# Optimization experiments

Hardware: AMD Instinct MI355X
Metric: run time of the kernel (lower is better)

The kernel has to match this reference:

```python
import jax, jax.numpy as jnp
import numpy as np

B, S, D = 2, 2048, 2048
H = 16
Q_LORA = 1024
KV_LORA = 512
NOPE = 128
ROPE = 64
VH = 128
QK = NOPE + ROPE
EPS = 1e-3
SCALE = QK ** -0.5


def rms_norm(x, w):
    x32 = x.astype(jnp.float32)
    n = x32 * jax.lax.rsqrt(jnp.mean(x32 * x32, axis=-1, keepdims=True) + EPS)
    return w * n.astype(x.dtype)


def apply_rope(x, cos, sin):
    # x: [b, s, h, d]; cos/sin: [1, s, 1, d//2].
    # torch view_as_complex pairs consecutive elements: (x0,x1),(x2,x3),...
    xr, xi = x[..., 0::2], x[..., 1::2]
    yr = xr * cos - xi * sin
    yi = xr * sin + xi * cos
    return jnp.stack([yr, yi], axis=-1).reshape(x.shape)


def setup_inputs() -> dict:
    key = jax.random.key(0)
    ks = jax.random.split(key, 8)

    def lin(k, out, inn):
        bound = 1.0 / float(np.sqrt(inn))
        return jax.random.uniform(k, (out, inn), jnp.float32, -bound, bound)

    inv_freq = 1.0 / (10000.0 ** (np.arange(0, ROPE, 2, dtype=np.float32) / ROPE))
    ang = np.arange(S, dtype=np.float32)[:, None] * inv_freq[None, :]  # [S, ROPE/2]
    return {
        "x": jax.random.normal(ks[0], (B, S, D), jnp.float32),
        "start_pos": 0,
        "cos": jnp.asarray(np.cos(ang), jnp.float32),
        "sin": jnp.asarray(np.sin(ang), jnp.float32),
        "wq_a_w": lin(ks[1], Q_LORA, D),
        "wq_a_b": jnp.zeros((Q_LORA,), jnp.float32),
        "q_norm_w": jnp.ones((Q_LORA,), jnp.float32),
        "wq_b_w": lin(ks[2], H * QK, Q_LORA),
        "wq_b_b": jnp.zeros((H * QK,), jnp.float32),
        "wkv_a_w": lin(ks[3], KV_LORA + ROPE, D),
        "wkv_a_b": jnp.zeros((KV_LORA + ROPE,), jnp.float32),
        "kv_norm_w": jnp.ones((KV_LORA,), jnp.float32),
        "wkv_b_w": lin(ks[4], H * (NOPE + VH), KV_LORA),
        "wo_w": lin(ks[5], D, H * VH),
        "wo_b": jnp.zeros((D,), jnp.float32),
    }


def reference(x, start_pos, cos, sin, wq_a_w, wq_a_b, q_norm_w, wq_b_w, wq_b_b,
              wkv_a_w, wkv_a_b, kv_norm_w, wkv_b_w, wo_w, wo_b):
    b, s, _ = x.shape
    cos_ = cos[None, :, None, :]
    sin_ = sin[None, :, None, :]

    # q path: low-rank down-proj, RMSNorm, up-proj
    q = rms_norm(x @ wq_a_w.T + wq_a_b, q_norm_w) @ wq_b_w.T + wq_b_b
    q = q.reshape(b, s, H, QK)
    q_nope, q_pe = q[..., :NOPE], q[..., NOPE:]
    q_pe = apply_rope(q_pe, cos_, sin_)

    # kv path: joint low-rank latent + rope key
    kv_full = x @ wkv_a_w.T + wkv_a_b
    kv, k_pe = kv_full[..., :KV_LORA], kv_full[..., KV_LORA:]
    k_pe = apply_rope(k_pe[:, :, None, :], cos_, sin_)[:, :, 0, :]  # [b, t, ROPE]

    wkv_b = wkv_b_w.reshape(H, NOPE + VH, KV_LORA)
    # absorb k up-projection into q (MLA trick): q_nope -> latent space
    q_nope = jnp.einsum('bshd,hdc->bshc', q_nope, wkv_b[:, :NOPE])  # [b,s,H,KV_LORA]

    kv_c = rms_norm(kv, kv_norm_w)  # latent KV cache contents [b, t, KV_LORA]

    scores = (jnp.einsum('bshc,btc->bsht', q_nope, kv_c)
              + jnp.einsum('bshr,btr->bsht', q_pe, k_pe)) * SCALE
    # NOTE: source builds a causal mask but never adds it -> plain softmax (faithful)
    probs = jax.nn.softmax(scores.astype(jnp.float32), axis=-1).astype(x.dtype)

    o = jnp.einsum('bsht,btc->bshc', probs, kv_c)          # latent output
    o = jnp.einsum('bshc,hdc->bshd', o, wkv_b[:, NOPE:])    # v up-projection
    return o.reshape(b, s, H * VH) @ wo_w.T + wo_b
```

## Files before the change

kernel.cpp:

```cpp
#include <hip/hip_runtime.h>
#include <stdint.h>

typedef uint16_t u16;
typedef __bf16 bf16x8 __attribute__((ext_vector_type(8)));
typedef float f32x4 __attribute__((ext_vector_type(4)));

#define EPS 1e-3f
#define SCALE_F 0.07216878364870323f
#define THR_RAW 110.0f

__device__ __forceinline__ float bf2f(u16 u) {
    union { uint32_t i; float f; } v; v.i = ((uint32_t)u) << 16; return v.f;
}
__device__ __forceinline__ u16 f2bf(float f) {
    union { float f; uint32_t i; } v; v.f = f;
    uint32_t x = v.i;
    return (u16)((x + 0x7fffu + ((x >> 16) & 1u)) >> 16);
}

__device__ __forceinline__ void async_cp16(const u16* g, u16* l) {
    __builtin_amdgcn_global_load_lds(
        (const __attribute__((address_space(1))) uint32_t*)g,
        (__attribute__((address_space(3))) uint32_t*)l,
        16, 0, 0);
}

struct Cvt {
    const void* src[14];
    u16* dst[14];
    long off[15];
};

__global__ __launch_bounds__(256) void cvt_kernel(Cvt c, const uint32_t* qnw_u32, long total8)
{
    const long i8 = (long)blockIdx.x * 256 + threadIdx.x;
    if (i8 >= total8) return;
    const long e = i8 * 8;
    const bool is_f32 = (qnw_u32[0] == 0x3F800000u);
    int t = 0;
    while (e >= c.off[t + 1]) ++t;
    const long local = e - c.off[t];
    u16* d = c.dst[t] + local;
    if (is_f32) {
        const float* s = (const float*)c.src[t] + local;
        #pragma unroll
        for (int j = 0; j < 8; ++j) d[j] = f2bf(s[j]);
    } else {
        const u16* s = (const u16*)c.src[t] + local;
        #pragma unroll
        for (int j = 0; j < 8; ++j) d[j] = s[j];
    }
}

__global__ __launch_bounds__(256) void gemm_bt_kernel(
    const u16* __restrict__ A, const u16* __restrict__ B,
    const u16* __restrict__ bias, u16* __restrict__ C,
    int M, int N, int K, int lda, int ldb, int ldc, float alpha, int c_f32,
    int z0, int hcnt,
    long sAl, long sAb, long sAh,
    long sBl, long sBb, long sBh,
    long sCl, long sCb, long sCh)
{
    const int zl = blockIdx.z;
    const int zg = z0 + zl;
    const int zb = zg / hcnt, zh = zg - zb * hcnt;
    A += (long)zl * sAl + (long)zb * sAb + (long)zh * sAh;
    B += (long)zl * sBl + (long)zb * sBb + (long)zh * sBh;
    C += (long)zl * sCl + (long)zb * sCb + (long)zh * sCh;

    __shared__ u16 As[128 * 64];
    __shared__ u16 Bs[128 * 64];

    const int tid  = threadIdx.x;
    const int wave = tid >> 6, lane = tid & 63;
    const int wm = (wave >> 1) << 6, wn = (wave & 1) << 6;
    const int quad = lane >> 4, r15 = lane & 15;

    const int tileM = blockIdx.y * 128;
    const int tileN = blockIdx.x * 128;

    const u16* Ag[4]; const u16* Bg[4];
    u16* lA[4]; u16* lB[4];
    #pragma unroll
    for (int i = 0; i < 4; ++i) {
        const int cc = i * 256 + tid;
        const int rA = cc >> 3, kb = (cc & 7) << 3;
        int rB = tileN + rA; if (rB > N - 1) rB = N - 1;
        Ag[i] = A + (long)(tileM + rA) * lda + kb;
        Bg[i] = B + (long)rB * ldb + kb;
        lA[i] = &As[cc << 3];
        lB[i] = &Bs[cc << 3];
    }

    f32x4 acc[4][4] = {};

    const u16* aRd[4]; const u16* bRd[4];
    #pragma unroll
    for (int i = 0; i < 4; ++i) {
        aRd[i] = &As[(wm + i * 16 + r15) * 64 + quad * 8];
        bRd[i] = &Bs[(wn + i * 16 + r15) * 64 + quad * 8];
    }

    for (int k0 = 0; k0 < K; k0 += 64) {
        #pragma unroll
        for (int i = 0; i < 4; ++i) {
            async_cp16(Ag[i], lA[i]);
            async_cp16(Bg[i], lB[i]);
            Ag[i] += 64; Bg[i] += 64;
        }
        __syncthreads();
        #pragma unroll
        for (int kk = 0; kk < 2; ++kk) {
            bf16x8 af[4], bfr[4];
            #pragma unroll
            for (int i = 0; i < 4; ++i) {
                af[i]  = *(const bf16x8*)(aRd[i] + kk * 32);
                bfr[i] = *(const bf16x8*)(bRd[i] + kk * 32);
            }
            #pragma unroll
            for (int mi = 0; mi < 4; ++mi)
                #pragma unroll
                for (int ni = 0; ni < 4; ++ni)
                    acc[mi][ni] = __builtin_amdgcn_mfma_f32_16x16x32_bf16(
                        af[mi], bfr[ni], acc[mi][ni], 0, 0, 0);
        }
        __syncthreads();
    }

    #pragma unroll
    for (int mi = 0; mi < 4; ++mi) {
        const int row = tileM + wm + mi * 16 + quad * 4;
        #pragma unroll
        for (int ni = 0; ni < 4; ++ni) {
            const int col = tileN + wn + ni * 16 + r15;
            if (col < N) {
                if (c_f32) {
                    const float bv = bias ? bf2f(bias[col]) : 0.f;
                    #pragma unroll
                    for (int r = 0; r < 4; ++r)
                        ((float*)C)[(long)(row + r) * ldc + col] =
                            acc[mi][ni][r] * alpha + bv;
                } else {
                    #pragma unroll
                    for (int r = 0; r < 4; ++r) {
                        u16 t = f2bf(acc[mi][ni][r] * alpha);
                        if (bias) t = f2bf(bf2f(t) + bf2f(bias[col]));
                        C[(long)(row + r) * ldc + col] = t;
                    }
                }
            }
        }
    }
}

#define PS 72

__global__ __launch_bounds__(256, 2) void flash_kernel(
    const u16* __restrict__ q, const u16* __restrict__ K2,
    const u16* __restrict__ Vt, u16* __restrict__ O)
{
    __shared__ __align__(16) u16 Ks[64 * 192];
    __shared__ __align__(16) u16 Vs[128 * 64];
    __shared__ __align__(16) u16 Ps[4][32 * PS];

    const int bid = blockIdx.x;
    const int xcd = bid & 7;
    const int idx = bid >> 3;
    const int bh  = xcd * 4 + (idx >> 4);
    const int mt  = idx & 15;
    const int b = bh >> 4, h = bh & 15;

    const int tid = threadIdx.x;
    const int wave = tid >> 6, lane = tid & 63;
    const int quad = lane >> 4, r15 = lane & 15;
    const int r7 = r15 & 7;

    const long qrow0 = (long)b * 2048 + mt * 128 + wave * 32;
    u16* myPs = Ps[wave];

    bf16x8 qf[2][6];
    #pragma unroll
    for (int mi = 0; mi < 2; ++mi) {
        const u16* qp = q + (qrow0 + mi * 16 + r15) * 3072 + h * 192 + quad * 8;
        #pragma unroll
        for (int kst = 0; kst < 6; ++kst)
            qf[mi][kst] = *(const bf16x8*)(qp + kst * 32);
    }

    f32x4 Oacc[2][8] = {};
    float m_i[2][4], l_i[2][4];
    #pragma unroll
    for (int mi = 0; mi < 2; ++mi)
        #pragma unroll
        for (int r = 0; r < 4; ++r) { m_i[mi][r] = -1e30f; l_i[mi][r] = 0.f; }

    const u16* Kbh = K2 + (long)b * 2048 * 3072 + h * 192;
    const u16* Vbh = Vt + (long)bh * 128 * 2048;

    const u16* gK[6];
    #pragma unroll
    for (int i = 0; i < 6; ++i) {
        const int c = i * 256 + tid;
        const int row = c / 24, s = c - row * 24;
        gK[i] = Kbh + (long)row * 3072 + ((s ^ (row & 7)) << 3);
    }
    const u16* gV[4];
    #pragma unroll
    for (int i = 0; i < 4; ++i) {
        const int c = i * 256 + tid;
        const int d = c >> 3, s = c & 7;
        gV[i] = Vbh + (long)d * 2048 + ((s ^ (d & 7)) << 3);
    }

    #pragma unroll
    for (int i = 0; i < 6; ++i) {
        async_cp16(gK[i], &Ks[(i * 256 + tid) << 3]);
        gK[i] += 64 * 3072;
    }
    __syncthreads();

    for (int j = 0; j < 32; ++j) {
        #pragma unroll
        for (int i = 0; i < 4; ++i) {
            async_cp16(gV[i], &Vs[(i * 256 + tid) << 3]);
            gV[i] += 64;
        }

        f32x4 S[2][4] = {};
        __builtin_amdgcn_s_setprio(1);
        #pragma unroll
        for (int kst = 0; kst < 6; ++kst) {
            bf16x8 bfr[4];
            #pragma unroll
            for (int ni = 0; ni < 4; ++ni)
                bfr[ni] = *(const bf16x8*)&Ks[(ni * 16 + r15) * 192
                                              + (((kst * 4 + quad) ^ r7) << 3)];
            #pragma unroll
            for (int mi = 0; mi < 2; ++mi)
                #pragma unroll
                for (int ni = 0; ni < 4; ++ni)
                    S[mi][ni] = __builtin_amdgcn_mfma_f32_16x16x32_bf16(
                        qf[mi][kst], bfr[ni], S[mi][ni], 0, 0, 0);
        }
        __builtin_amdgcn_s_setprio(0);

        __syncthreads();

        #pragma unroll
        for (int i = 0; i < 6; ++i) {
            async_cp16(gK[i], &Ks[(i * 256 + tid) << 3]);
            gK[i] += 64 * 3072;
        }

        float tmax[2][4];
        float gmax = -1e30f;
        #pragma unroll
        for (int mi = 0; mi < 2; ++mi)
            #pragma unroll
            for (int r = 0; r < 4; ++r) {
                float t = S[mi][0][r];
                #pragma unroll
                for (int ni = 1; ni < 4; ++ni) t = fmaxf(t, S[mi][ni][r]);
                t = fmaxf(t, __shfl_xor(t, 1, 16));
                t = fmaxf(t, __shfl_xor(t, 2, 16));
                t = fmaxf(t, __shfl_xor(t, 4, 16));
                t = fmaxf(t, __shfl_xor(t, 8, 16));
                tmax[mi][r] = t;
                gmax = fmaxf(gmax, t - m_i[mi][r]);
            }
        if (!__all(gmax <= THR_RAW)) {
            #pragma unroll
            for (int mi = 0; mi < 2; ++mi)
                #pragma unroll
                for (int r = 0; r < 4; ++r) {
                    const float mnew = fmaxf(m_i[mi][r], tmax[mi][r]);
                    const float al = __expf((m_i[mi][r] - mnew) * SCALE_F);
                    m_i[mi][r] = mnew;
                    l_i[mi][r] *= al;
                    #pragma unroll
                    for (int ni = 0; ni < 8; ++ni) Oacc[mi][ni][r] *= al;
                }
        }
        #pragma unroll
        for (int mi = 0; mi < 2; ++mi)
            #pragma unroll
            for (int r = 0; r < 4; ++r) {
                const int lrow = mi * 16 + quad * 4 + r;
                const float mm = m_i[mi][r];
                float ps = 0.f;
                #pragma unroll
                for (int ni = 0; ni < 4; ++ni) {
                    const float pv = __expf((S[mi][ni][r] - mm) * SCALE_F);
                    ps += pv;
                    myPs[lrow * PS + ni * 16 + r15] = f2bf(pv);
                }
                ps += __shfl_xor(ps, 1, 16);
                ps += __shfl_xor(ps, 2, 16);
                ps += __shfl_xor(ps, 4, 16);
                ps += __shfl_xor(ps, 8, 16);
                l_i[mi][r] += ps;
            }

        __builtin_amdgcn_s_setprio(1);
        #pragma unroll
        for (int kst = 0; kst < 2; ++kst) {
            bf16x8 af[2], bv[8];
            #pragma unroll
            for (int mi = 0; mi < 2; ++mi)
                af[mi] = *(const bf16x8*)&myPs[(mi * 16 + r15) * PS
                                               + kst * 32 + quad * 8];
            #pragma unroll
            for (int ni = 0; ni < 8; ++ni)
                bv[ni] = *(const bf16x8*)&Vs[(ni * 16 + r15) * 64
                                             + (((kst * 4 + quad) ^ r7) << 3)];
            #pragma unroll
            for (int mi = 0; mi < 2; ++mi)
                #pragma unroll
                for (int ni = 0; ni < 8; ++ni)
                    Oacc[mi][ni] = __builtin_amdgcn_mfma_f32_16x16x32_bf16(
                        af[mi], bv[ni], Oacc[mi][ni], 0, 0, 0);
        }
        __builtin_amdgcn_s_setprio(0);

        __syncthreads();
    }

    #pragma unroll
    for (int mi = 0; mi < 2; ++mi)
        #pragma unroll
        for (int r = 0; r < 4; ++r) {
            const float inv = 1.f / l_i[mi][r];
            const long row = qrow0 + mi * 16 + quad * 4 + r;
            #pragma unroll
            for (int ni = 0; ni < 8; ++ni)
                O[row * 2048 + h * 128 + ni * 16 + r15] =
                    f2bf(Oacc[mi][ni][r] * inv);
        }
}

__global__ __launch_bounds__(256) void rmsnorm_kernel(
    const u16* __restrict__ x, const u16* __restrict__ w, u16* __restrict__ y, int n)
{
    const long row = blockIdx.x;
    const u16* xr = x + row * n;
    u16* yr = y + row * n;
    const int tid = threadIdx.x;
    const int cnt = n >> 8;
    float v[4];
    float ss = 0.f;
    for (int i = 0; i < cnt; ++i) { v[i] = bf2f(xr[tid + (i << 8)]); ss += v[i] * v[i]; }
    for (int o = 32; o; o >>= 1) ss += __shfl_xor(ss, o, 64);
    __shared__ float sm[4];
    if ((tid & 63) == 0) sm[tid >> 6] = ss;
    __syncthreads();
    const float rinv = rsqrtf((sm[0] + sm[1] + sm[2] + sm[3]) / (float)n + EPS);
    for (int i = 0; i < cnt; ++i) {
        const u16 nb = f2bf(v[i] * rinv);
        yr[tid + (i << 8)] = f2bf(bf2f(w[tid + (i << 8)]) * bf2f(nb));
    }
}

__global__ __launch_bounds__(256) void kv_kernel(
    const u16* __restrict__ cosb, const u16* __restrict__ sinb,
    const u16* __restrict__ w, u16* __restrict__ kvf)
{
    const long bs = blockIdx.x;
    const int s = (int)(bs & 2047);
    u16* io = kvf + bs * 576;
    const int tid = threadIdx.x;
    const float v0 = bf2f(io[tid * 2]), v1 = bf2f(io[tid * 2 + 1]);
    float ss = v0 * v0 + v1 * v1;
    for (int off = 32; off; off >>= 1) ss += __shfl_xor(ss, off, 64);
    __shared__ float sm[4];
    if ((tid & 63) == 0) sm[tid >> 6] = ss;
    __syncthreads();
    const float rinv = rsqrtf((sm[0] + sm[1] + sm[2] + sm[3]) / 512.f + EPS);
    const u16 n0 = f2bf(v0 * rinv), n1 = f2bf(v1 * rinv);
    io[tid * 2]     = f2bf(bf2f(w[tid * 2]) * bf2f(n0));
    io[tid * 2 + 1] = f2bf(bf2f(w[tid * 2 + 1]) * bf2f(n1));
    if (tid < 32) {
        const int j = tid;
        const float xr = bf2f(io[512 + 2 * j]), xi = bf2f(io[512 + 2 * j + 1]);
        const float c = bf2f(cosb[s * 32 + j]), si = bf2f(sinb[s * 32 + j]);
        io[512 + 2 * j]     = f2bf(bf2f(f2bf(xr * c))  - bf2f(f2bf(xi * si)));
        io[512 + 2 * j + 1] = f2bf(bf2f(f2bf(xr * si)) + bf2f(f2bf(xi * c)));
    }
}

__global__ __launch_bounds__(256) void rope_q_kernel(
    const u16* __restrict__ cosb, const u16* __restrict__ sinb, u16* __restrict__ q)
{
    const int idx = blockIdx.x * 256 + threadIdx.x;
    const int j = idx & 31;
    const int h = (idx >> 5) & 15;
    const int bs = idx >> 9;
    const int s = bs & 2047;
    u16* p = q + (long)bs * 3072 + h * 192 + 128 + 2 * j;
    const float xr = bf2f(p[0]), xi = bf2f(p[1]);
    const float c = bf2f(cosb[s * 32 + j]), si = bf2f(sinb[s * 32 + j]);
    p[0] = f2bf(bf2f(f2bf(xr * c))  - bf2f(f2bf(xi * si)));
    p[1] = f2bf(bf2f(f2bf(xr * si)) + bf2f(f2bf(xi * c)));
}

__global__ __launch_bounds__(256) void k2rope_kernel(
    const u16* __restrict__ kvf, u16* __restrict__ K2)
{
    const long row = blockIdx.x;
    const int tid = threadIdx.x;
    #pragma unroll
    for (int i = 0; i < 4; ++i) {
        const int slot = tid + (i << 8);
        const int h = slot >> 6, r = slot & 63;
        K2[row * 3072 + h * 192 + 128 + r] = kvf[row * 576 + 512 + r];
    }
}

extern "C" void kernel_launch(void* const* d_in, const int* in_sizes, int n_in,
                              void* d_out, int out_size, void* d_ws, size_t ws_size,
                              hipStream_t stream)
{
    float* out = (float*)d_out;

    char* p = (char*)d_ws;
    auto alloc = [&](size_t elems) { u16* r = (u16*)p; p += elems * 2; return r; };
    u16* c_cos  = alloc(65536);
    u16* c_sin  = alloc(65536);
    u16* c_wqa  = alloc(2097152);
    u16* c_wqab = alloc(1024);
    u16* c_qnw  = alloc(1024);
    u16* c_wqb  = alloc(3145728);
    u16* c_wqbb = alloc(3072);
    u16* c_wkva = alloc(1179648);
    u16* c_wkvab= alloc(576);
    u16* c_kvnw = alloc(512);
    u16* c_wkvb = alloc(2097152);
    u16* c_wo   = alloc(4194304);
    u16* c_wob  = alloc(2048);
    u16* q   = alloc(4096UL * 3072);
    u16* kvf = alloc(4096UL * 576);
    u16* K2  = alloc(4096UL * 3072);
    u16* O   = alloc(4096UL * 2048);
    u16* q_a = (u16*)p;
    u16* xb = (u16*)d_out;
    u16* Vt = (u16*)d_out + 8388608;

    Cvt cv;
    const long sizes[14] = {8388608, 65536, 65536, 2097152, 1024, 1024, 3145728,
                            3072, 1179648, 576, 512, 2097152, 4194304, 2048};
    u16* dsts[14] = {xb, c_cos, c_sin, c_wqa, c_wqab, c_qnw, c_wqb, c_wqbb,
                     c_wkva, c_wkvab, c_kvnw, c_wkvb, c_wo, c_wob};
    const int srcidx[14] = {0, 2, 3, 4, 5, 6, 7, 8, 9, 10, 11, 12, 13, 14};
    long acc_off = 0;
    for (int t = 0; t < 14; ++t) {
        cv.src[t] = d_in[srcidx[t]];
        cv.dst[t] = dsts[t];
        cv.off[t] = acc_off;
        acc_off += sizes[t];
    }
    cv.off[14] = acc_off;
    const long total8 = acc_off / 8;
    cvt_kernel<<<dim3((unsigned)((total8 + 255) / 256)), dim3(256), 0, stream>>>(
        cv, (const uint32_t*)d_in[6], total8);

    auto gemm = [&](const u16* A, const u16* B, const u16* bias, u16* C,
                    int M, int N, int K, int lda, int ldb, int ldc, float alpha,
                    int c_f32, int nz, int z0, int hcnt,
                    long sAl, long sAb, long sAh,
                    long sBl, long sBb, long sBh,
                    long sCl, long sCb, long sCh) {
        dim3 grid((N + 127) / 128, M / 128, nz);
        gemm_bt_kernel<<<grid, dim3(256), 0, stream>>>(
            A, B, bias, C, M, N, K, lda, ldb, ldc, alpha, c_f32, z0, hcnt,
            sAl, sAb, sAh, sBl, sBb, sBh, sCl, sCb, sCh);
    };

    gemm(xb, c_wqa, c_wqab, q_a, 4096, 1024, 2048, 2048, 2048, 1024, 1.f, 0,
         1, 0, 1, 0, 0, 0, 0, 0, 0, 0, 0, 0);
    rmsnorm_kernel<<<4096, 256, 0, stream>>>(q_a, c_qnw, q_a, 1024);
    gemm(q_a, c_wqb, c_wqbb, q, 4096, 3072, 1024, 1024, 1024, 3072, 1.f, 0,
         1, 0, 1, 0, 0, 0, 0, 0, 0, 0, 0, 0);
    gemm(xb, c_wkva, c_wkvab, kvf, 4096, 576, 2048, 2048, 2048, 576, 1.f, 0,
         1, 0, 1, 0, 0, 0, 0, 0, 0, 0, 0, 0);
    kv_kernel<<<4096, 256, 0, stream>>>(c_cos, c_sin, c_kvnw, kvf);
    rope_q_kernel<<<8192, 256, 0, stream>>>(c_cos, c_sin, q);
    gemm(kvf, c_wkvb, nullptr, K2, 4096, 128, 512, 576, 512, 3072, 1.f, 0,
         16, 0, 16, 0, 0, 0, 0, 0, 256L * 512, 0, 0, 192);
    k2rope_kernel<<<4096, 256, 0, stream>>>(kvf, K2);
    gemm(c_wkvb + 128 * 512, kvf, nullptr, Vt, 128, 2048, 512, 512, 576, 2048, 1.f, 0,
         32, 0, 16,
         0, 0, 256L * 512,
         0, 2048L * 576, 0,
         0, 16L * 128 * 2048, 128L * 2048);
    flash_kernel<<<dim3(512), dim3(256), 0, stream>>>(q, K2, Vt, O);
    gemm(O, c_wo, c_wob, (u16*)out, 4096, 2048, 2048, 2048, 2048, 2048, 1.f, 1,
         1, 0, 1, 0, 0, 0, 0, 0, 0, 0, 0, 0);
}
```

Before: 574.4 us.

## Fuse q/kv down-projections, fold rope into flash and kv kernels, shrink flash tile

Places the wq_a and wkv_a weights next to each other so one GEMM (N=1600) produces both the q latent and the kv latent into a combined buffer. The rope_q and k2rope kernels are removed: q rope is now applied while loading q fragments inside flash_kernel, and kv_kernel writes the rotated key straight into K2. The flash kernel now gives each wave 16 query rows instead of 32 and launches twice as many blocks, which lowers register pressure and improves occupancy at the cost of less K/V reuse per block. The net effect is fewer launches and less memory traffic, traded against a smaller attention tile.

```diff
diff --git a/kernel.cpp b/kernel.cpp
--- a/kernel.cpp
+++ b/kernel.cpp
@@ -4,6 +4,7 @@
 typedef uint16_t u16;
 typedef __bf16 bf16x8 __attribute__((ext_vector_type(8)));
 typedef float f32x4 __attribute__((ext_vector_type(4)));
+typedef u16 u16x8 __attribute__((ext_vector_type(8)));
 
 #define EPS 1e-3f
 #define SCALE_F 0.07216878364870323f
@@ -157,17 +158,18 @@
 
 __global__ __launch_bounds__(256, 2) void flash_kernel(
     const u16* __restrict__ q, const u16* __restrict__ K2,
-    const u16* __restrict__ Vt, u16* __restrict__ O)
+    const u16* __restrict__ Vt, u16* __restrict__ O,
+    const u16* __restrict__ cosb, const u16* __restrict__ sinb)
 {
     __shared__ __align__(16) u16 Ks[64 * 192];
     __shared__ __align__(16) u16 Vs[128 * 64];
-    __shared__ __align__(16) u16 Ps[4][32 * PS];
+    __shared__ __align__(16) u16 Ps[4][16 * PS];
 
     const int bid = blockIdx.x;
     const int xcd = bid & 7;
     const int idx = bid >> 3;
-    const int bh  = xcd * 4 + (idx >> 4);
-    const int mt  = idx & 15;
+    const int bh  = xcd * 4 + (idx >> 5);
+    const int mt  = idx & 31;
     const int b = bh >> 4, h = bh & 15;
 
     const int tid = threadIdx.x;
@@ -175,24 +177,37 @@
     const int quad = lane >> 4, r15 = lane & 15;
     const int r7 = r15 & 7;
 
-    const long qrow0 = (long)b * 2048 + mt * 128 + wave * 32;
+    const long qrow0 = (long)b * 2048 + mt * 64 + wave * 16;
+    const int srow = (int)(qrow0 & 2047) + r15;
     u16* myPs = Ps[wave];
 
-    bf16x8 qf[2][6];
-    #pragma unroll
-    for (int mi = 0; mi < 2; ++mi) {
-        const u16* qp = q + (qrow0 + mi * 16 + r15) * 3072 + h * 192 + quad * 8;
-        #pragma unroll
-        for (int kst = 0; kst < 6; ++kst)
-            qf[mi][kst] = *(const bf16x8*)(qp + kst * 32);
-    }
-
-    f32x4 Oacc[2][8] = {};
-    float m_i[2][4], l_i[2][4];
-    #pragma unroll
-    for (int mi = 0; mi < 2; ++mi)
-        #pragma unroll
-        for (int r = 0; r < 4; ++r) { m_i[mi][r] = -1e30f; l_i[mi][r] = 0.f; }
+    bf16x8 qf[6];
+    {
+        const u16* qp = q + (qrow0 + r15) * 3072 + h * 192 + quad * 8;
+        #pragma unroll
+        for (int kst = 0; kst < 4; ++kst)
+            qf[kst] = *(const bf16x8*)(qp + kst * 32);
+        #pragma unroll
+        for (int kst = 4; kst < 6; ++kst) {
+            const u16x8 v = *(const u16x8*)(qp + kst * 32);
+            u16x8 o;
+            const int jj0 = (kst - 4) * 16 + quad * 4;
+            #pragma unroll
+            for (int pp = 0; pp < 4; ++pp) {
+                const float xr = bf2f(v[2 * pp]), xi = bf2f(v[2 * pp + 1]);
+                const float c  = bf2f(cosb[(long)srow * 32 + jj0 + pp]);
+                const float si = bf2f(sinb[(long)srow * 32 + jj0 + pp]);
+                o[2 * pp]     = f2bf(bf2f(f2bf(xr * c))  - bf2f(f2bf(xi * si)));
+                o[2 * pp + 1] = f2bf(bf2f(f2bf(xr * si)) + bf2f(f2bf(xi * c)));
+            }
+            qf[kst] = *(const bf16x8*)&o;
+        }
+    }
+
+    f32x4 Oacc[8] = {};
+    float m_i[4], l_i[4];
+    #pragma unroll
+    for (int r = 0; r < 4; ++r) { m_i[r] = -1e30f; l_i[r] = 0.f; }
 
     const u16* Kbh = K2 + (long)b * 2048 * 3072 + h * 192;
     const u16* Vbh = Vt + (long)bh * 128 * 2048;
@@ -221,12 +236,14 @@
 
     for (int j = 0; j < 32; ++j) {
         #pragma unroll
-        for (int i = 0; i < 4; ++i) {
+        for (int i = 0; i < 4; ++i)
             async_cp16(gV[i], &Vs[(i * 256 + tid) << 3]);
-            gV[i] += 64;
-        }
-
-        f32x4 S[2][4] = {};
+        if (j < 31) {
+            #pragma unroll
+            for (int i = 0; i < 4; ++i) gV[i] += 64;
+        }
+
+        f32x4 S[4] = {};
         __builtin_amdgcn_s_setprio(1);
         #pragma unroll
         for (int kst = 0; kst < 6; ++kst) {
@@ -236,11 +253,9 @@
                 bfr[ni] = *(const bf16x8*)&Ks[(ni * 16 + r15) * 192
                                               + (((kst * 4 + quad) ^ r7) << 3)];
             #pragma unroll
-            for (int mi = 0; mi < 2; ++mi)
-                #pragma unroll
-                for (int ni = 0; ni < 4; ++ni)
-                    S[mi][ni] = __builtin_amdgcn_mfma_f32_16x16x32_bf16(
-                        qf[mi][kst], bfr[ni], S[mi][ni], 0, 0, 0);
+            for (int ni = 0; ni < 4; ++ni)
+                S[ni] = __builtin_amdgcn_mfma_f32_16x16x32_bf16(
+                    qf[kst], bfr[ni], S[ni], 0, 0, 0);
         }
         __builtin_amdgcn_s_setprio(0);
 
@@ -252,73 +267,62 @@
             gK[i] += 64 * 3072;
         }
 
-        float tmax[2][4];
+        float tmax[4];
         float gmax = -1e30f;
         #pragma unroll
-        for (int mi = 0; mi < 2; ++mi)
+        for (int r = 0; r < 4; ++r) {
+            float t = S[0][r];
+            #pragma unroll
+            for (int ni = 1; ni < 4; ++ni) t = fmaxf(t, S[ni][r]);
+            t = fmaxf(t, __shfl_xor(t, 1, 16));
+            t = fmaxf(t, __shfl_xor(t, 2, 16));
+            t = fmaxf(t, __shfl_xor(t, 4, 16));
+            t = fmaxf(t, __shfl_xor(t, 8, 16));
+            tmax[r] = t;
+            gmax = fmaxf(gmax, t - m_i[r]);
+        }
+        if (!__all(gmax <= THR_RAW)) {
             #pragma unroll
             for (int r = 0; r < 4; ++r) {
-                float t = S[mi][0][r];
+                const float mnew = fmaxf(m_i[r], tmax[r]);
+                const float al = __expf((m_i[r] - mnew) * SCALE_F);
+                m_i[r] = mnew;
+                l_i[r] *= al;
                 #pragma unroll
-                for (int ni = 1; ni < 4; ++ni) t = fmaxf(t, S[mi][ni][r]);
-                t = fmaxf(t, __shfl_xor(t, 1, 16));
-                t = fmaxf(t, __shfl_xor(t, 2, 16));
-                t = fmaxf(t, __shfl_xor(t, 4, 16));
-                t = fmaxf(t, __shfl_xor(t, 8, 16));
-                tmax[mi][r] = t;
-                gmax = fmaxf(gmax, t - m_i[mi][r]);
+                for (int ni = 0; ni < 8; ++ni) Oacc[ni][r] *= al;
             }
-        if (!__all(gmax <= THR_RAW)) {
-            #pragma unroll
-            for (int mi = 0; mi < 2; ++mi)
-                #pragma unroll
-                for (int r = 0; r < 4; ++r) {
-                    const float mnew = fmaxf(m_i[mi][r], tmax[mi][r]);
-                    const float al = __expf((m_i[mi][r] - mnew) * SCALE_F);
-                    m_i[mi][r] = mnew;
-                    l_i[mi][r] *= al;
-                    #pragma unroll
-                    for (int ni = 0; ni < 8; ++ni) Oacc[mi][ni][r] *= al;
-                }
-        }
-        #pragma unroll
-        for (int mi = 0; mi < 2; ++mi)
-            #pragma unroll
-            for (int r = 0; r < 4; ++r) {
-                const int lrow = mi * 16 + quad * 4 + r;
-                const float mm = m_i[mi][r];
-                float ps = 0.f;
-                #pragma unroll
-                for (int ni = 0; ni < 4; ++ni) {
-                    const float pv = __expf((S[mi][ni][r] - mm) * SCALE_F);
-                    ps += pv;
-                    myPs[lrow * PS + ni * 16 + r15] = f2bf(pv);
-                }
-                ps += __shfl_xor(ps, 1, 16);
-                ps += __shfl_xor(ps, 2, 16);
-                ps += __shfl_xor(ps, 4, 16);
-                ps += __shfl_xor(ps, 8, 16);
-                l_i[mi][r] += ps;
+        }
+        #pragma unroll
+        for (int r = 0; r < 4; ++r) {
+            const int lrow = quad * 4 + r;
+            const float mm = m_i[r];
+            float ps = 0.f;
+            #pragma unroll
+            for (int ni = 0; ni < 4; ++ni) {
+                const float pv = __expf((S[ni][r] - mm) * SCALE_F);
+                ps += pv;
+                myPs[lrow * PS + ni * 16 + r15] = f2bf(pv);
             }
+            ps += __shfl_xor(ps, 1, 16);
+            ps += __shfl_xor(ps, 2, 16);
+            ps += __shfl_xor(ps, 4, 16);
+            ps += __shfl_xor(ps, 8, 16);
+            l_i[r] += ps;
+        }
 
         __builtin_amdgcn_s_setprio(1);
         #pragma unroll
         for (int kst = 0; kst < 2; ++kst) {
-            bf16x8 af[2], bv[8];
-            #pragma unroll
-            for (int mi = 0; mi < 2; ++mi)
-                af[mi] = *(const bf16x8*)&myPs[(mi * 16 + r15) * PS
-                                               + kst * 32 + quad * 8];
+            bf16x8 af, bv[8];
+            af = *(const bf16x8*)&myPs[r15 * PS + kst * 32 + quad * 8];
             #pragma unroll
             for (int ni = 0; ni < 8; ++ni)
                 bv[ni] = *(const bf16x8*)&Vs[(ni * 16 + r15) * 64
                                              + (((kst * 4 + quad) ^ r7) << 3)];
             #pragma unroll
-            for (int mi = 0; mi < 2; ++mi)
-                #pragma unroll
-                for (int ni = 0; ni < 8; ++ni)
-                    Oacc[mi][ni] = __builtin_amdgcn_mfma_f32_16x16x32_bf16(
-                        af[mi], bv[ni], Oacc[mi][ni], 0, 0, 0);
+            for (int ni = 0; ni < 8; ++ni)
+                Oacc[ni] = __builtin_amdgcn_mfma_f32_16x16x32_bf16(
+                    af, bv[ni], Oacc[ni], 0, 0, 0);
         }
         __builtin_amdgcn_s_setprio(0);
 
@@ -326,24 +330,23 @@
     }
 
     #pragma unroll
-    for (int mi = 0; mi < 2; ++mi)
-        #pragma unroll
-        for (int r = 0; r < 4; ++r) {
-            const float inv = 1.f / l_i[mi][r];
-            const long row = qrow0 + mi * 16 + quad * 4 + r;
-            #pragma unroll
-            for (int ni = 0; ni < 8; ++ni)
-                O[row * 2048 + h * 128 + ni * 16 + r15] =
-                    f2bf(Oacc[mi][ni][r] * inv);
-        }
+    for (int r = 0; r < 4; ++r) {
+        const float inv = 1.f / l_i[r];
+        const long row = qrow0 + quad * 4 + r;
+        #pragma unroll
+        for (int ni = 0; ni < 8; ++ni)
+            O[row * 2048 + h * 128 + ni * 16 + r15] =
+                f2bf(Oacc[ni][r] * inv);
+    }
 }
 
 __global__ __launch_bounds__(256) void rmsnorm_kernel(
-    const u16* __restrict__ x, const u16* __restrict__ w, u16* __restrict__ y, int n)
+    const u16* __restrict__ x, const u16* __restrict__ w, u16* __restrict__ y,
+    int n, int ldx)
 {
     const long row = blockIdx.x;
-    const u16* xr = x + row * n;
-    u16* yr = y + row * n;
+    const u16* xr = x + row * ldx;
+    u16* yr = y + row * ldx;
     const int tid = threadIdx.x;
     const int cnt = n >> 8;
     float v[4];
@@ -362,16 +365,17 @@
 
 __global__ __launch_bounds__(256) void kv_kernel(
     const u16* __restrict__ cosb, const u16* __restrict__ sinb,
-    const u16* __restrict__ w, u16* __restrict__ kvf)
+    const u16* __restrict__ w, u16* __restrict__ comb, u16* __restrict__ K2)
 {
     const long bs = blockIdx.x;
     const int s = (int)(bs & 2047);
-    u16* io = kvf + bs * 576;
+    u16* io = comb + bs * 1600 + 1024;
     const int tid = threadIdx.x;
     const float v0 = bf2f(io[tid * 2]), v1 = bf2f(io[tid * 2 + 1]);
     float ss = v0 * v0 + v1 * v1;
     for (int off = 32; off; off >>= 1) ss += __shfl_xor(ss, off, 64);
     __shared__ float sm[4];
+    __shared__ u16 rp[64];
     if ((tid & 63) == 0) sm[tid >> 6] = ss;
     __syncthreads();
     const float rinv = rsqrtf((sm[0] + sm[1] + sm[2] + sm[3]) / 512.f + EPS);
@@ -382,36 +386,15 @@
         const int j = tid;
         const float xr = bf2f(io[512 + 2 * j]), xi = bf2f(io[512 + 2 * j + 1]);
         const float c = bf2f(cosb[s * 32 + j]), si = bf2f(sinb[s * 32 + j]);
-        io[512 + 2 * j]     = f2bf(bf2f(f2bf(xr * c))  - bf2f(f2bf(xi * si)));
-        io[512 + 2 * j + 1] = f2bf(bf2f(f2bf(xr * si)) + bf2f(f2bf(xi * c)));
-    }
-}
-
-__global__ __launch_bounds__(256) void rope_q_kernel(
-    const u16* __restrict__ cosb, const u16* __restrict__ sinb, u16* __restrict__ q)
-{
-    const int idx = blockIdx.x * 256 + threadIdx.x;
-    const int j = idx & 31;
-    const int h = (idx >> 5) & 15;
-    const int bs = idx >> 9;
-    const int s = bs & 2047;
-    u16* p = q + (long)bs * 3072 + h * 192 + 128 + 2 * j;
-    const float xr = bf2f(p[0]), xi = bf2f(p[1]);
-    const float c = bf2f(cosb[s * 32 + j]), si = bf2f(sinb[s * 32 + j]);
-    p[0] = f2bf(bf2f(f2bf(xr * c))  - bf2f(f2bf(xi * si)));
-    p[1] = f2bf(bf2f(f2bf(xr * si)) + bf2f(f2bf(xi * c)));
-}
-
-__global__ __launch_bounds__(256) void k2rope_kernel(
-    const u16* __restrict__ kvf, u16* __restrict__ K2)
-{
-    const long row = blockIdx.x;
-    const int tid = threadIdx.x;
+        rp[2 * j]     = f2bf(bf2f(f2bf(xr * c))  - bf2f(f2bf(xi * si)));
+        rp[2 * j + 1] = f2bf(bf2f(f2bf(xr * si)) + bf2f(f2bf(xi * c)));
+    }
+    __syncthreads();
     #pragma unroll
     for (int i = 0; i < 4; ++i) {
         const int slot = tid + (i << 8);
         const int h = slot >> 6, r = slot & 63;
-        K2[row * 3072 + h * 192 + 128 + r] = kvf[row * 576 + 512 + r];
+        K2[bs * 3072 + h * 192 + 128 + r] = rp[r];
     }
 }
 
@@ -426,21 +409,20 @@
     u16* c_cos  = alloc(65536);
     u16* c_sin  = alloc(65536);
     u16* c_wqa  = alloc(2097152);
+    u16* c_wkva = alloc(1179648);
     u16* c_wqab = alloc(1024);
+    u16* c_wkvab= alloc(576);
     u16* c_qnw  = alloc(1024);
     u16* c_wqb  = alloc(3145728);
     u16* c_wqbb = alloc(3072);
-    u16* c_wkva = alloc(1179648);
-    u16* c_wkvab= alloc(576);
     u16* c_kvnw = alloc(512);
     u16* c_wkvb = alloc(2097152);
     u16* c_wo   = alloc(4194304);
     u16* c_wob  = alloc(2048);
-    u16* q   = alloc(4096UL * 3072);
-    u16* kvf = alloc(4096UL * 576);
-    u16* K2  = alloc(4096UL * 3072);
-    u16* O   = alloc(4096UL * 2048);
-    u16* q_a = (u16*)p;
+    u16* q    = alloc(4096UL * 3072);
+    u16* K2   = alloc(4096UL * 3072);
+    u16* O    = alloc(4096UL * 2048);
+    u16* comb = alloc(4096UL * 1600);
     u16* xb = (u16*)d_out;
     u16* Vt = (u16*)d_out + 8388608;
 
@@ -474,24 +456,21 @@
             sAl, sAb, sAh, sBl, sBb, sBh, sCl, sCb, sCh);
     };
 
-    gemm(xb, c_wqa, c_wqab, q_a, 4096, 1024, 2048, 2048, 2048, 1024, 1.f, 0,
+    gemm(xb, c_wqa, c_wqab, comb, 4096, 1600, 2048, 2048, 2048, 1600, 1.f, 0,
          1, 0, 1, 0, 0, 0, 0, 0, 0, 0, 0, 0);
-    rmsnorm_kernel<<<4096, 256, 0, stream>>>(q_a, c_qnw, q_a, 1024);
-    gemm(q_a, c_wqb, c_wqbb, q, 4096, 3072, 1024, 1024, 1024, 3072, 1.f, 0,
+    rmsnorm_kernel<<<4096, 256, 0, stream>>>(comb, c_qnw, comb, 1024, 1600);
+    gemm(comb, c_wqb, c_wqbb, q, 4096, 3072, 1024, 1600, 1024, 3072, 1.f, 0,
          1, 0, 1, 0, 0, 0, 0, 0, 0, 0, 0, 0);
-    gemm(xb, c_wkva, c_wkvab, kvf, 4096, 576, 2048, 2048, 2048, 576, 1.f, 0,
-         1, 0, 1, 0, 0, 0, 0, 0, 0, 0, 0, 0);
-    kv_kernel<<<4096, 256, 0, stream>>>(c_cos, c_sin, c_kvnw, kvf);
-    rope_q_kernel<<<8192, 256, 0, stream>>>(c_cos, c_sin, q);
-    gemm(kvf, c_wkvb, nullptr, K2, 4096, 128, 512, 576, 512, 3072, 1.f, 0,
+    kv_kernel<<<4096, 256, 0, stream>>>(c_cos, c_sin, c_kvnw, comb, K2);
+    gemm(comb + 1024, c_wkvb, nullptr, K2, 4096, 128, 512, 1600, 512, 3072, 1.f, 0,
          16, 0, 16, 0, 0, 0, 0, 0, 256L * 512, 0, 0, 192);
-    k2rope_kernel<<<4096, 256, 0, stream>>>(kvf, K2);
-    gemm(c_wkvb + 128 * 512, kvf, nullptr, Vt, 128, 2048, 512, 512, 576, 2048, 1.f, 0,
+    gemm(c_wkvb + 128 * 512, comb + 1024, nullptr, Vt, 128, 2048, 512, 512, 1600, 2048,
+         1.f, 0,
          32, 0, 16,
          0, 0, 256L * 512,
-         0, 2048L * 576, 0,
+         0, 2048L * 1600, 0,
          0, 16L * 128 * 2048, 128L * 2048);
-    flash_kernel<<<dim3(512), dim3(256), 0, stream>>>(q, K2, Vt, O);
+    flash_kernel<<<dim3(1024), dim3(256), 0, stream>>>(q, K2, Vt, O, c_cos, c_sin);
     gemm(O, c_wo, c_wob, (u16*)out, 4096, 2048, 2048, 2048, 2048, 2048, 1.f, 1,
          1, 0, 1, 0, 0, 0, 0, 0, 0, 0, 0, 0);
 }
```

Result: faster. 559.2 us (-2.7%).

## Merge q/kv down-projection GEMMs and fuse RoPE into flash and kv kernels

Applied to the files above, without the earlier changes.

The x@wq_a and x@wkv_a projections become one GEMM with N=1600, made possible by placing the two weight matrices next to each other in the workspace. The output goes into a combined buffer that later stages read through larger leading dimensions. Query RoPE now runs inside the flash kernel while it loads q fragments, which removes the separate rope_q pass over q. The k_pe copy into K2 moves into kv_kernel, removing two kernel launches and their extra global memory passes. In exchange, the flash kernel prologue does more scalar work and cos/sin loads, and the strided 1600-wide buffer may change GEMM alignment or efficiency.

```diff
diff --git a/kernel.cpp b/kernel.cpp
--- a/kernel.cpp
+++ b/kernel.cpp
@@ -4,6 +4,7 @@
 typedef uint16_t u16;
 typedef __bf16 bf16x8 __attribute__((ext_vector_type(8)));
 typedef float f32x4 __attribute__((ext_vector_type(4)));
+typedef u16 u16x8 __attribute__((ext_vector_type(8)));
 
 #define EPS 1e-3f
 #define SCALE_F 0.07216878364870323f
@@ -157,7 +158,8 @@
 
 __global__ __launch_bounds__(256, 2) void flash_kernel(
     const u16* __restrict__ q, const u16* __restrict__ K2,
-    const u16* __restrict__ Vt, u16* __restrict__ O)
+    const u16* __restrict__ Vt, u16* __restrict__ O,
+    const u16* __restrict__ cosb, const u16* __restrict__ sinb)
 {
     __shared__ __align__(16) u16 Ks[64 * 192];
     __shared__ __align__(16) u16 Vs[128 * 64];
@@ -183,8 +185,24 @@
     for (int mi = 0; mi < 2; ++mi) {
         const u16* qp = q + (qrow0 + mi * 16 + r15) * 3072 + h * 192 + quad * 8;
         #pragma unroll
-        for (int kst = 0; kst < 6; ++kst)
+        for (int kst = 0; kst < 4; ++kst)
             qf[mi][kst] = *(const bf16x8*)(qp + kst * 32);
+        const int srow = mt * 128 + wave * 32 + mi * 16 + r15;
+        #pragma unroll
+        for (int kst = 4; kst < 6; ++kst) {
+            const u16x8 v = *(const u16x8*)(qp + kst * 32);
+            u16x8 o;
+            const int jj0 = (kst - 4) * 16 + quad * 4;
+            #pragma unroll
+            for (int pp = 0; pp < 4; ++pp) {
+                const float xr = bf2f(v[2 * pp]), xi = bf2f(v[2 * pp + 1]);
+                const float c  = bf2f(cosb[(long)srow * 32 + jj0 + pp]);
+                const float si = bf2f(sinb[(long)srow * 32 + jj0 + pp]);
+                o[2 * pp]     = f2bf(bf2f(f2bf(xr * c))  - bf2f(f2bf(xi * si)));
+                o[2 * pp + 1] = f2bf(bf2f(f2bf(xr * si)) + bf2f(f2bf(xi * c)));
+            }
+            qf[mi][kst] = *(const bf16x8*)&o;
+        }
     }
 
     f32x4 Oacc[2][8] = {};
@@ -339,11 +357,12 @@
 }
 
 __global__ __launch_bounds__(256) void rmsnorm_kernel(
-    const u16* __restrict__ x, const u16* __restrict__ w, u16* __restrict__ y, int n)
+    const u16* __restrict__ x, const u16* __restrict__ w, u16* __restrict__ y,
+    int n, int ldx)
 {
     const long row = blockIdx.x;
-    const u16* xr = x + row * n;
-    u16* yr = y + row * n;
+    const u16* xr = x + row * ldx;
+    u16* yr = y + row * ldx;
     const int tid = threadIdx.x;
     const int cnt = n >> 8;
     float v[4];
@@ -362,16 +381,17 @@
 
 __global__ __launch_bounds__(256) void kv_kernel(
     const u16* __restrict__ cosb, const u16* __restrict__ sinb,
-    const u16* __restrict__ w, u16* __restrict__ kvf)
+    const u16* __restrict__ w, u16* __restrict__ comb, u16* __restrict__ K2)
 {
     const long bs = blockIdx.x;
     const int s = (int)(bs & 2047);
-    u16* io = kvf + bs * 576;
+    u16* io = comb + bs * 1600 + 1024;
     const int tid = threadIdx.x;
     const float v0 = bf2f(io[tid * 2]), v1 = bf2f(io[tid * 2 + 1]);
     float ss = v0 * v0 + v1 * v1;
     for (int off = 32; off; off >>= 1) ss += __shfl_xor(ss, off, 64);
     __shared__ float sm[4];
+    __shared__ u16 rp[64];
     if ((tid & 63) == 0) sm[tid >> 6] = ss;
     __syncthreads();
     const float rinv = rsqrtf((sm[0] + sm[1] + sm[2] + sm[3]) / 512.f + EPS);
@@ -382,36 +402,15 @@
         const int j = tid;
         const float xr = bf2f(io[512 + 2 * j]), xi = bf2f(io[512 + 2 * j + 1]);
         const float c = bf2f(cosb[s * 32 + j]), si = bf2f(sinb[s * 32 + j]);
-        io[512 + 2 * j]     = f2bf(bf2f(f2bf(xr * c))  - bf2f(f2bf(xi * si)));
-        io[512 + 2 * j + 1] = f2bf(bf2f(f2bf(xr * si)) + bf2f(f2bf(xi * c)));
-    }
-}
-
-__global__ __launch_bounds__(256) void rope_q_kernel(
-    const u16* __restrict__ cosb, const u16* __restrict__ sinb, u16* __restrict__ q)
-{
-    const int idx = blockIdx.x * 256 + threadIdx.x;
-    const int j = idx & 31;
-    const int h = (idx >> 5) & 15;
-    const int bs = idx >> 9;
-    const int s = bs & 2047;
-    u16* p = q + (long)bs * 3072 + h * 192 + 128 + 2 * j;
-    const float xr = bf2f(p[0]), xi = bf2f(p[1]);
-    const float c = bf2f(cosb[s * 32 + j]), si = bf2f(sinb[s * 32 + j]);
-    p[0] = f2bf(bf2f(f2bf(xr * c))  - bf2f(f2bf(xi * si)));
-    p[1] = f2bf(bf2f(f2bf(xr * si)) + bf2f(f2bf(xi * c)));
-}
-
-__global__ __launch_bounds__(256) void k2rope_kernel(
-    const u16* __restrict__ kvf, u16* __restrict__ K2)
-{
-    const long row = blockIdx.x;
-    const int tid = threadIdx.x;
+        rp[2 * j]     = f2bf(bf2f(f2bf(xr * c))  - bf2f(f2bf(xi * si)));
+        rp[2 * j + 1] = f2bf(bf2f(f2bf(xr * si)) + bf2f(f2bf(xi * c)));
+    }
+    __syncthreads();
     #pragma unroll
     for (int i = 0; i < 4; ++i) {
         const int slot = tid + (i << 8);
         const int h = slot >> 6, r = slot & 63;
-        K2[row * 3072 + h * 192 + 128 + r] = kvf[row * 576 + 512 + r];
+        K2[bs * 3072 + h * 192 + 128 + r] = rp[r];
     }
 }
 
@@ -426,21 +425,20 @@
     u16* c_cos  = alloc(65536);
     u16* c_sin  = alloc(65536);
     u16* c_wqa  = alloc(2097152);
+    u16* c_wkva = alloc(1179648);
     u16* c_wqab = alloc(1024);
+    u16* c_wkvab= alloc(576);
     u16* c_qnw  = alloc(1024);
     u16* c_wqb  = alloc(3145728);
     u16* c_wqbb = alloc(3072);
-    u16* c_wkva = alloc(1179648);
-    u16* c_wkvab= alloc(576);
     u16* c_kvnw = alloc(512);
     u16* c_wkvb = alloc(2097152);
     u16* c_wo   = alloc(4194304);
     u16* c_wob  = alloc(2048);
-    u16* q   = alloc(4096UL * 3072);
-    u16* kvf = alloc(4096UL * 576);
-    u16* K2  = alloc(4096UL * 3072);
-    u16* O   = alloc(4096UL * 2048);
-    u16* q_a = (u16*)p;
+    u16* q    = alloc(4096UL * 3072);
+    u16* K2   = alloc(4096UL * 3072);
+    u16* O    = alloc(4096UL * 2048);
+    u16* comb = alloc(4096UL * 1600);
     u16* xb = (u16*)d_out;
     u16* Vt = (u16*)d_out + 8388608;
 
@@ -474,24 +472,21 @@
             sAl, sAb, sAh, sBl, sBb, sBh, sCl, sCb, sCh);
     };
 
-    gemm(xb, c_wqa, c_wqab, q_a, 4096, 1024, 2048, 2048, 2048, 1024, 1.f, 0,
+    gemm(xb, c_wqa, c_wqab, comb, 4096, 1600, 2048, 2048, 2048, 1600, 1.f, 0,
          1, 0, 1, 0, 0, 0, 0, 0, 0, 0, 0, 0);
-    rmsnorm_kernel<<<4096, 256, 0, stream>>>(q_a, c_qnw, q_a, 1024);
-    gemm(q_a, c_wqb, c_wqbb, q, 4096, 3072, 1024, 1024, 1024, 3072, 1.f, 0,
+    rmsnorm_kernel<<<4096, 256, 0, stream>>>(comb, c_qnw, comb, 1024, 1600);
+    gemm(comb, c_wqb, c_wqbb, q, 4096, 3072, 1024, 1600, 1024, 3072, 1.f, 0,
          1, 0, 1, 0, 0, 0, 0, 0, 0, 0, 0, 0);
-    gemm(xb, c_wkva, c_wkvab, kvf, 4096, 576, 2048, 2048, 2048, 576, 1.f, 0,
-         1, 0, 1, 0, 0, 0, 0, 0, 0, 0, 0, 0);
-    kv_kernel<<<4096, 256, 0, stream>>>(c_cos, c_sin, c_kvnw, kvf);
-    rope_q_kernel<<<8192, 256, 0, stream>>>(c_cos, c_sin, q);
-    gemm(kvf, c_wkvb, nullptr, K2, 4096, 128, 512, 576, 512, 3072, 1.f, 0,
+    kv_kernel<<<4096, 256, 0, stream>>>(c_cos, c_sin, c_kvnw, comb, K2);
+    gemm(comb + 1024, c_wkvb, nullptr, K2, 4096, 128, 512, 1600, 512, 3072, 1.f, 0,
          16, 0, 16, 0, 0, 0, 0, 0, 256L * 512, 0, 0, 192);
-    k2rope_kernel<<<4096, 256, 0, stream>>>(kvf, K2);
-    gemm(c_wkvb + 128 * 512, kvf, nullptr, Vt, 128, 2048, 512, 512, 576, 2048, 1.f, 0,
+    gemm(c_wkvb + 128 * 512, comb + 1024, nullptr, Vt, 128, 2048, 512, 512, 1600, 2048,
+         1.f, 0,
          32, 0, 16,
          0, 0, 256L * 512,
-         0, 2048L * 576, 0,
+         0, 2048L * 1600, 0,
          0, 16L * 128 * 2048, 128L * 2048);
-    flash_kernel<<<dim3(512), dim3(256), 0, stream>>>(q, K2, Vt, O);
+    flash_kernel<<<dim3(512), dim3(256), 0, stream>>>(q, K2, Vt, O, c_cos, c_sin);
     gemm(O, c_wo, c_wob, (u16*)out, 4096, 2048, 2048, 2048, 2048, 2048, 1.f, 1,
          1, 0, 1, 0, 0, 0, 0, 0, 0, 0, 0, 0);
 }
```

New measurement: 529.8 us. 7.8% less time.
